# Performance work log

Hardware: AMD Instinct MI355X
Metric: run time of the kernel (lower is better)

The kernel has to match this reference:

```python
import jax, jax.numpy as jnp
import numpy as np

N_NODES = 50000
N_EDGES = 800000
D_IN = 1024
D_OUT = 256
LEAKY_SLOPE = 0.01  # F.leaky_relu default


def setup_inputs() -> dict:
    key = jax.random.key(0)
    k_x, k_w, k_b, k_src, k_dst, k_ew, k_norm = jax.random.split(key, 7)
    x = jax.random.normal(k_x, (N_NODES, D_IN), dtype=jnp.float32)
    # xavier_uniform-style scale for the weight
    limit = np.sqrt(6.0 / (D_IN + D_OUT)).astype(np.float32)
    weight = jax.random.uniform(k_w, (D_IN, D_OUT), dtype=jnp.float32, minval=-limit, maxval=limit)
    stdv = 1.0 / np.sqrt(D_OUT)
    bias = jax.random.uniform(k_b, (D_OUT,), dtype=jnp.float32, minval=-stdv, maxval=stdv)
    src = jax.random.randint(k_src, (N_EDGES,), 0, N_NODES, dtype=jnp.int64)
    dst = jax.random.randint(k_dst, (N_EDGES,), 0, N_NODES, dtype=jnp.int64)
    edge_index = jnp.stack([src, dst], axis=0)  # [2, E]
    edge_weight = jax.random.uniform(k_ew, (N_EDGES,), dtype=jnp.float32)
    norm = jax.random.uniform(k_norm, (N_NODES, 1), dtype=jnp.float32) + 0.5  # avoid div-by-~0
    return {"x": x, "weight": weight, "bias": bias, "edge_index": edge_index,
            "edge_weight": edge_weight, "norm": norm}


def reference(x, weight, bias, edge_index, edge_weight, norm):
    # support = input @ W            [N, D_OUT]
    support = x @ weight
    src = edge_index[0]
    dst = edge_index[1]
    # spmm(adj, support): out[i] = sum_{e: dst_e == i} w_e * support[src_e]
    msgs = support[src] * edge_weight[:, None]            # [E, D_OUT]
    out = jax.ops.segment_sum(msgs, dst, num_segments=x.shape[0])  # [N, D_OUT]
    out = out / norm + bias
    return jax.nn.leaky_relu(out, negative_slope=LEAKY_SLOPE)
```

## Files before the change

### kernel.cpp

```cpp
#include <hip/hip_runtime.h>
#include <hip/hip_bf16.h>

#define N_NODES 50000
#define N_EDGES 800000
#define D_IN    1024
#define D_OUT   256
#define CAP     64
#define LEAKY   0.01f

typedef __attribute__((ext_vector_type(8))) short bf16x8;
typedef __attribute__((ext_vector_type(4))) float f32x4;
typedef __attribute__((ext_vector_type(4))) int   i32x4;
typedef unsigned short u16;

__device__ __forceinline__ u16 f2bfu(float f) {
  uint32_t x = __float_as_uint(f);
  uint32_t r = (x + 0x7FFFu + ((x >> 16) & 1u)) >> 16;
  return (u16)r;
}
__device__ __forceinline__ float bfu2f(u16 u) {
  return __uint_as_float(((uint32_t)u) << 16);
}
__device__ __forceinline__ int swz(int b) { return b ^ (((b >> 7) & 7) << 4); }
__device__ __forceinline__ int paddr(int r, int c) {
  return swz(((r) >> 1) * 128 + ((r) & 1) * 64 + (c));
}

__device__ __forceinline__ void gll16(const void* g, void* l) {
  __builtin_amdgcn_global_load_lds(
      (const __attribute__((address_space(1))) uint32_t*)g,
      (__attribute__((address_space(3))) uint32_t*)l, 16, 0, 0);
}

__global__ __launch_bounds__(256) void wconv_kernel(const float* __restrict__ w,
                                                    char* __restrict__ img,
                                                    int* __restrict__ deg) {
  const int t = blockIdx.x * 256 + threadIdx.x;
  if (t < N_NODES) deg[t] = 0;
  const int t2 = t + 32768;
  if (t2 < N_NODES) deg[t2] = 0;

  const int n   = t & 255;
  const int kc  = (t >> 8) * 8;
  const int kt  = kc >> 5;
  const int kin = kc & 31;
  bf16x8 v;
#pragma unroll
  for (int i = 0; i < 8; ++i) v[i] = (short)f2bfu(w[(size_t)(kc + i) * D_OUT + n]);
  *(bf16x8*)(img + kt * 16384 + paddr(n, kin * 2)) = v;
}

#define BMg 256
#define GEMM_BLOCKS ((N_NODES + BMg - 1) / BMg)
#define BUILD_BLOCKS 60

__global__ __launch_bounds__(512) void gemm_build_kernel(
    const float* __restrict__ x, const char* __restrict__ img,
    u16* __restrict__ support,
    const int* __restrict__ ei, const float* __restrict__ ew,
    int* __restrict__ deg, int2* __restrict__ csr) {
  __shared__ u16 Wbuf[3][8192];
  __shared__ u16 Xbuf[3][8192];

  if (blockIdx.x < BUILD_BLOCKS) {
    const int t0 = blockIdx.x * 512 + threadIdx.x;
    for (int e = t0; e < N_EDGES; e += BUILD_BLOCKS * 512) {
      const int src = ei[e];
      const int dst = ei[N_EDGES + e];
      const float w = ew[e];
      const int slot = atomicAdd(&deg[dst], 1);
      if (slot < CAP) csr[dst * CAP + slot] = make_int2(src, __float_as_int(w));
    }
    return;
  }

  const int tid  = threadIdx.x;
  const int lane = tid & 63;
  const int wid  = tid >> 6;
  const int wn   = wid & 1;
  const int wm   = wid >> 1;
  const int l15  = lane & 15;
  const int l16  = lane >> 4;
  const int m0   = (blockIdx.x - BUILD_BLOCKS) * BMg;

  f32x4 acc[8][4];
#pragma unroll
  for (int i = 0; i < 8; ++i)
#pragma unroll
    for (int j = 0; j < 4; ++j) acc[i][j] = (f32x4)0.0f;

  const int xrow = tid >> 1;
  const int xkc  = (tid & 1) * 16;
  const int xrg  = min(m0 + xrow, N_NODES - 1);
  const float* xp = x + (size_t)xrg * D_IN + xkc;
  const int xw0 = paddr(xrow, xkc * 2);
  const int xw1 = paddr(xrow, xkc * 2 + 16);

  int a_off[8], b_off[4];
#pragma unroll
  for (int nf = 0; nf < 8; ++nf)
    a_off[nf] = paddr(wn * 128 + nf * 16 + l15, l16 * 16);
#pragma unroll
  for (int mf = 0; mf < 4; ++mf)
    b_off[mf] = paddr(wm * 64 + mf * 16 + l15, l16 * 16);

  f32x4 xr[2][4];

#define XLOAD(set, tile) do {                                              \
    const int kcl_ = min((tile), 31);                                      \
    const float* p_ = xp + kcl_ * 32;                                      \
    xr[set][0] = __builtin_nontemporal_load((const f32x4*)(p_));           \
    xr[set][1] = __builtin_nontemporal_load((const f32x4*)(p_ + 4));       \
    xr[set][2] = __builtin_nontemporal_load((const f32x4*)(p_ + 8));       \
    xr[set][3] = __builtin_nontemporal_load((const f32x4*)(p_ + 12));      \
  } while (0)

#define GLL(sl, tile) do {                                                 \
    const int kcl_ = min((tile), 31);                                      \
    gll16(img + kcl_ * 16384 + tid * 16, (char*)&Wbuf[sl][0] + tid * 16);  \
    gll16(img + kcl_ * 16384 + 8192 + tid * 16,                            \
          (char*)&Wbuf[sl][0] + 8192 + tid * 16);                          \
  } while (0)

#define XCVT(set, sl) do {                                                 \
    bf16x8 v0_, v1_;                                                       \
    v0_[0] = (short)f2bfu(xr[set][0][0]); v0_[1] = (short)f2bfu(xr[set][0][1]); \
    v0_[2] = (short)f2bfu(xr[set][0][2]); v0_[3] = (short)f2bfu(xr[set][0][3]); \
    v0_[4] = (short)f2bfu(xr[set][1][0]); v0_[5] = (short)f2bfu(xr[set][1][1]); \
    v0_[6] = (short)f2bfu(xr[set][1][2]); v0_[7] = (short)f2bfu(xr[set][1][3]); \
    v1_[0] = (short)f2bfu(xr[set][2][0]); v1_[1] = (short)f2bfu(xr[set][2][1]); \
    v1_[2] = (short)f2bfu(xr[set][2][2]); v1_[3] = (short)f2bfu(xr[set][2][3]); \
    v1_[4] = (short)f2bfu(xr[set][3][0]); v1_[5] = (short)f2bfu(xr[set][3][1]); \
    v1_[6] = (short)f2bfu(xr[set][3][2]); v1_[7] = (short)f2bfu(xr[set][3][3]); \
    *(bf16x8*)((char*)&Xbuf[sl][0] + xw0) = v0_;                           \
    *(bf16x8*)((char*)&Xbuf[sl][0] + xw1) = v1_;                           \
  } while (0)

#define MFMA_TILE(sl) do {                                                 \
    bf16x8 af_[8], bf_[4];                                                 \
    _Pragma("unroll")                                                      \
    for (int nf_ = 0; nf_ < 8; ++nf_)                                      \
      af_[nf_] = *(const bf16x8*)((const char*)&Wbuf[sl][0] + a_off[nf_]); \
    _Pragma("unroll")                                                      \
    for (int mf_ = 0; mf_ < 4; ++mf_)                                      \
      bf_[mf_] = *(const bf16x8*)((const char*)&Xbuf[sl][0] + b_off[mf_]); \
    _Pragma("unroll")                                                      \
    for (int nf_ = 0; nf_ < 8; ++nf_)                                      \
      _Pragma("unroll")                                                    \
      for (int mf_ = 0; mf_ < 4; ++mf_)                                    \
        acc[nf_][mf_] = __builtin_amdgcn_mfma_f32_16x16x32_bf16(           \
            af_[nf_], bf_[mf_], acc[nf_][mf_], 0, 0, 0);                   \
  } while (0)

#define SYNC() do {                                                        \
    asm volatile("s_waitcnt vmcnt(6)" ::: "memory");                       \
    __builtin_amdgcn_sched_barrier(0);                                     \
    asm volatile("s_waitcnt lgkmcnt(0)" ::: "memory");                     \
    __builtin_amdgcn_s_barrier();                                          \
  } while (0)

#define BODY(sA, sB, sC, eN, eC, kt) do {                                  \
    MFMA_TILE(sA);                                                         \
    XCVT(eC, sB);                                                          \
    XLOAD(eN, (kt) + 2);                                                   \
    GLL(sC, (kt) + 2);                                                     \
    SYNC();                                                                \
  } while (0)

  XLOAD(0, 0);
  GLL(0, 0);
  XLOAD(1, 1);
  GLL(1, 1);
  XCVT(0, 0);
  asm volatile("s_waitcnt vmcnt(6)" ::: "memory");
  __builtin_amdgcn_sched_barrier(0);
  asm volatile("s_waitcnt lgkmcnt(0)" ::: "memory");
  __builtin_amdgcn_s_barrier();

  for (int kt = 0; kt < 30; kt += 6) {
    BODY(0, 1, 2, 0, 1, kt);
    BODY(1, 2, 0, 1, 0, kt + 1);
    BODY(2, 0, 1, 0, 1, kt + 2);
    BODY(0, 1, 2, 1, 0, kt + 3);
    BODY(1, 2, 0, 0, 1, kt + 4);
    BODY(2, 0, 1, 1, 0, kt + 5);
  }
  BODY(0, 1, 2, 0, 1, 30);
  BODY(1, 2, 0, 1, 0, 31);

#undef XLOAD
#undef GLL
#undef XCVT
#undef MFMA_TILE
#undef SYNC
#undef BODY

#pragma unroll
  for (int mf = 0; mf < 4; ++mf) {
    const int m = m0 + wm * 64 + mf * 16 + l15;
    if (m < N_NODES) {
#pragma unroll
      for (int nf = 0; nf < 8; ++nf) {
        const int n = wn * 128 + nf * 16 + l16 * 4;
        ushort4 o;
        o.x = f2bfu(acc[nf][mf][0]);
        o.y = f2bfu(acc[nf][mf][1]);
        o.z = f2bfu(acc[nf][mf][2]);
        o.w = f2bfu(acc[nf][mf][3]);
        *(ushort4*)&support[(size_t)m * D_OUT + n] = o;
      }
    }
  }
}

__global__ __launch_bounds__(256) void agg_kernel(const u16* __restrict__ support,
                                                  const int* __restrict__ deg,
                                                  const int2* __restrict__ csr,
                                                  const float* __restrict__ norm,
                                                  const float* __restrict__ bias,
                                                  float* __restrict__ out) {
  const int lane = threadIdx.x & 63;
  const int wid  = threadIdx.x >> 6;
  const int node = blockIdx.x * 4 + wid;
  const int d    = min(deg[node], CAP);
  const int cb   = node * CAP;
  const int ch   = lane * 4;

  float a0 = 0.f, a1 = 0.f, a2 = 0.f, a3 = 0.f;
  int s = 0;

  for (; s + 16 <= d; s += 16) {
    i32x4 q[8];
#pragma unroll
    for (int i = 0; i < 8; ++i)
      q[i] = __builtin_nontemporal_load((const i32x4*)&csr[cb + s + 2 * i]);
    ushort4 v[16];
#pragma unroll
    for (int i = 0; i < 8; ++i) {
      v[2 * i]     = *(const ushort4*)&support[(size_t)q[i][0] * D_OUT + ch];
      v[2 * i + 1] = *(const ushort4*)&support[(size_t)q[i][2] * D_OUT + ch];
    }
#pragma unroll
    for (int i = 0; i < 8; ++i) {
      const float wa = __int_as_float(q[i][1]);
      const float wb = __int_as_float(q[i][3]);
      a0 = fmaf(wa, bfu2f(v[2 * i].x), a0);
      a1 = fmaf(wa, bfu2f(v[2 * i].y), a1);
      a2 = fmaf(wa, bfu2f(v[2 * i].z), a2);
      a3 = fmaf(wa, bfu2f(v[2 * i].w), a3);
      a0 = fmaf(wb, bfu2f(v[2 * i + 1].x), a0);
      a1 = fmaf(wb, bfu2f(v[2 * i + 1].y), a1);
      a2 = fmaf(wb, bfu2f(v[2 * i + 1].z), a2);
      a3 = fmaf(wb, bfu2f(v[2 * i + 1].w), a3);
    }
  }

  for (; s + 8 <= d; s += 8) {
    i32x4 q[4];
#pragma unroll
    for (int i = 0; i < 4; ++i)
      q[i] = __builtin_nontemporal_load((const i32x4*)&csr[cb + s + 2 * i]);
    ushort4 v[8];
#pragma unroll
    for (int i = 0; i < 4; ++i) {
      v[2 * i]     = *(const ushort4*)&support[(size_t)q[i][0] * D_OUT + ch];
      v[2 * i + 1] = *(const ushort4*)&support[(size_t)q[i][2] * D_OUT + ch];
    }
#pragma unroll
    for (int i = 0; i < 4; ++i) {
      const float wa = __int_as_float(q[i][1]);
      const float wb = __int_as_float(q[i][3]);
      a0 = fmaf(wa, bfu2f(v[2 * i].x), a0);
      a1 = fmaf(wa, bfu2f(v[2 * i].y), a1);
      a2 = fmaf(wa, bfu2f(v[2 * i].z), a2);
      a3 = fmaf(wa, bfu2f(v[2 * i].w), a3);
      a0 = fmaf(wb, bfu2f(v[2 * i + 1].x), a0);
      a1 = fmaf(wb, bfu2f(v[2 * i + 1].y), a1);
      a2 = fmaf(wb, bfu2f(v[2 * i + 1].z), a2);
      a3 = fmaf(wb, bfu2f(v[2 * i + 1].w), a3);
    }
  }

  for (; s < d; ++s) {
    const int2  e   = csr[cb + s];
    const float wgt = __int_as_float(e.y);
    const ushort4 v = *(const ushort4*)&support[(size_t)e.x * D_OUT + ch];
    a0 = fmaf(wgt, bfu2f(v.x), a0);
    a1 = fmaf(wgt, bfu2f(v.y), a1);
    a2 = fmaf(wgt, bfu2f(v.z), a2);
    a3 = fmaf(wgt, bfu2f(v.w), a3);
  }

  const float rn = 1.0f / norm[node];
  const float4 b = *(const float4*)&bias[ch];
  float o0 = fmaf(a0, rn, b.x);
  float o1 = fmaf(a1, rn, b.y);
  float o2 = fmaf(a2, rn, b.z);
  float o3 = fmaf(a3, rn, b.w);
  o0 = o0 > 0.f ? o0 : o0 * LEAKY;
  o1 = o1 > 0.f ? o1 : o1 * LEAKY;
  o2 = o2 > 0.f ? o2 : o2 * LEAKY;
  o3 = o3 > 0.f ? o3 : o3 * LEAKY;
  f32x4 ov;
  ov[0] = o0; ov[1] = o1; ov[2] = o2; ov[3] = o3;
  __builtin_nontemporal_store(ov, (f32x4*)&out[(size_t)node * D_OUT + ch]);
}

extern "C" void kernel_launch(void* const* d_in, const int* in_sizes, int n_in,
                              void* d_out, int out_size, void* d_ws, size_t ws_size,
                              hipStream_t stream) {
  const float* x    = (const float*)d_in[0];
  const float* w    = (const float*)d_in[1];
  const float* bias = (const float*)d_in[2];
  const int*   ei   = (const int*)d_in[3];
  const float* ew   = (const float*)d_in[4];
  const float* norm = (const float*)d_in[5];
  float* out = (float*)d_out;

  char* ws = (char*)d_ws;
  u16*   support = (u16*)  (ws);
  char*  img     =         (ws + 25600000);
  int2*  csr     = (int2*) (ws + 26124288);
  int*   deg     = (int*)  (ws + 51724288);

  wconv_kernel<<<128, 256, 0, stream>>>(w, img, deg);
  gemm_build_kernel<<<BUILD_BLOCKS + GEMM_BLOCKS, 512, 0, stream>>>(
      x, img, support, ei, ew, deg, csr);
  agg_kernel<<<N_NODES / 4, 256, 0, stream>>>(support, deg, csr, norm, bias, out);
}
```

Baseline: 187.2 us.

## Restructure GEMM pipeline to 64-wide K tiles with double buffering and ping-pong barriers

Doubles the K tile from 32 to 64 and changes the weight image and LDS layout to match. The triple-buffered pipeline becomes a double buffer, and each tile's MFMA work is split into four quarters, each wrapped in s_barrier, s_setprio(1) and a second barrier. X loads are interleaved between the quarters. The aim is fewer synchronization rounds per K and better overlap of global loads with MFMA issue, at the cost of more barriers per tile, full vmcnt(0) waits, and more LDS (128KB total).

Measured after the change: 275.0 us. +46.9%, slower.

```diff
diff --git a/kernel.cpp b/kernel.cpp
--- a/kernel.cpp
+++ b/kernel.cpp
@@ -22,9 +22,6 @@
   return __uint_as_float(((uint32_t)u) << 16);
 }
 __device__ __forceinline__ int swz(int b) { return b ^ (((b >> 7) & 7) << 4); }
-__device__ __forceinline__ int paddr(int r, int c) {
-  return swz(((r) >> 1) * 128 + ((r) & 1) * 64 + (c));
-}
 
 __device__ __forceinline__ void gll16(const void* g, void* l) {
   __builtin_amdgcn_global_load_lds(
@@ -35,19 +32,19 @@
 __global__ __launch_bounds__(256) void wconv_kernel(const float* __restrict__ w,
                                                     char* __restrict__ img,
                                                     int* __restrict__ deg) {
-  const int t = blockIdx.x * 256 + threadIdx.x;
+  const int t   = blockIdx.x * 256 + threadIdx.x;
   if (t < N_NODES) deg[t] = 0;
   const int t2 = t + 32768;
   if (t2 < N_NODES) deg[t2] = 0;
 
   const int n   = t & 255;
   const int kc  = (t >> 8) * 8;
-  const int kt  = kc >> 5;
-  const int kin = kc & 31;
+  const int kt  = kc >> 6;
+  const int kin = kc & 63;
   bf16x8 v;
 #pragma unroll
   for (int i = 0; i < 8; ++i) v[i] = (short)f2bfu(w[(size_t)(kc + i) * D_OUT + n]);
-  *(bf16x8*)(img + kt * 16384 + paddr(n, kin * 2)) = v;
+  *(bf16x8*)(img + kt * 32768 + swz(n * 128 + kin * 2)) = v;
 }
 
 #define BMg 256
@@ -59,8 +56,8 @@
     u16* __restrict__ support,
     const int* __restrict__ ei, const float* __restrict__ ew,
     int* __restrict__ deg, int2* __restrict__ csr) {
-  __shared__ u16 Wbuf[3][8192];
-  __shared__ u16 Xbuf[3][8192];
+  __shared__ u16 Wb[2][16384];
+  __shared__ u16 Xb[2][16384];
 
   if (blockIdx.x < BUILD_BLOCKS) {
     const int t0 = blockIdx.x * 512 + threadIdx.x;
@@ -89,111 +86,129 @@
 #pragma unroll
     for (int j = 0; j < 4; ++j) acc[i][j] = (f32x4)0.0f;
 
-  const int xrow = tid >> 1;
-  const int xkc  = (tid & 1) * 16;
-  const int xrg  = min(m0 + xrow, N_NODES - 1);
-  const float* xp = x + (size_t)xrg * D_IN + xkc;
-  const int xw0 = paddr(xrow, xkc * 2);
-  const int xw1 = paddr(xrow, xkc * 2 + 16);
-
-  int a_off[8], b_off[4];
-#pragma unroll
-  for (int nf = 0; nf < 8; ++nf)
-    a_off[nf] = paddr(wn * 128 + nf * 16 + l15, l16 * 16);
-#pragma unroll
-  for (int mf = 0; mf < 4; ++mf)
-    b_off[mf] = paddr(wm * 64 + mf * 16 + l15, l16 * 16);
-
-  f32x4 xr[2][4];
-
-#define XLOAD(set, tile) do {                                              \
-    const int kcl_ = min((tile), 31);                                      \
-    const float* p_ = xp + kcl_ * 32;                                      \
-    xr[set][0] = __builtin_nontemporal_load((const f32x4*)(p_));           \
-    xr[set][1] = __builtin_nontemporal_load((const f32x4*)(p_ + 4));       \
-    xr[set][2] = __builtin_nontemporal_load((const f32x4*)(p_ + 8));       \
-    xr[set][3] = __builtin_nontemporal_load((const f32x4*)(p_ + 12));      \
-  } while (0)
-
-#define GLL(sl, tile) do {                                                 \
-    const int kcl_ = min((tile), 31);                                      \
-    gll16(img + kcl_ * 16384 + tid * 16, (char*)&Wbuf[sl][0] + tid * 16);  \
-    gll16(img + kcl_ * 16384 + 8192 + tid * 16,                            \
-          (char*)&Wbuf[sl][0] + 8192 + tid * 16);                          \
-  } while (0)
-
-#define XCVT(set, sl) do {                                                 \
-    bf16x8 v0_, v1_;                                                       \
-    v0_[0] = (short)f2bfu(xr[set][0][0]); v0_[1] = (short)f2bfu(xr[set][0][1]); \
-    v0_[2] = (short)f2bfu(xr[set][0][2]); v0_[3] = (short)f2bfu(xr[set][0][3]); \
-    v0_[4] = (short)f2bfu(xr[set][1][0]); v0_[5] = (short)f2bfu(xr[set][1][1]); \
-    v0_[6] = (short)f2bfu(xr[set][1][2]); v0_[7] = (short)f2bfu(xr[set][1][3]); \
-    v1_[0] = (short)f2bfu(xr[set][2][0]); v1_[1] = (short)f2bfu(xr[set][2][1]); \
-    v1_[2] = (short)f2bfu(xr[set][2][2]); v1_[3] = (short)f2bfu(xr[set][2][3]); \
-    v1_[4] = (short)f2bfu(xr[set][3][0]); v1_[5] = (short)f2bfu(xr[set][3][1]); \
-    v1_[6] = (short)f2bfu(xr[set][3][2]); v1_[7] = (short)f2bfu(xr[set][3][3]); \
-    *(bf16x8*)((char*)&Xbuf[sl][0] + xw0) = v0_;                           \
-    *(bf16x8*)((char*)&Xbuf[sl][0] + xw1) = v1_;                           \
-  } while (0)
-
-#define MFMA_TILE(sl) do {                                                 \
-    bf16x8 af_[8], bf_[4];                                                 \
+  const int xrow  = tid >> 1;
+  const int xhalf = (tid & 1) * 32;
+  const int xrg   = min(m0 + xrow, N_NODES - 1);
+  const float* xp = x + (size_t)xrg * D_IN + xhalf;
+  int xw[4];
+#pragma unroll
+  for (int j = 0; j < 4; ++j) xw[j] = swz(xrow * 128 + (xhalf + j * 8) * 2);
+
+  int a_off[2][8], b_off[2][4];
+#pragma unroll
+  for (int ks = 0; ks < 2; ++ks) {
+#pragma unroll
+    for (int nf = 0; nf < 8; ++nf)
+      a_off[ks][nf] = swz((wn * 128 + nf * 16 + l15) * 128 + ks * 64 + l16 * 16);
+#pragma unroll
+    for (int mf = 0; mf < 4; ++mf)
+      b_off[ks][mf] = swz((wm * 64 + mf * 16 + l15) * 128 + ks * 64 + l16 * 16);
+  }
+
+  f32x4 xs[8];
+  bf16x8 af[8];
+
+#define XLD(i0, tt) do {                                                   \
+    const int kc_ = min((tt), 15);                                         \
+    xs[i0]     = __builtin_nontemporal_load((const f32x4*)(xp + kc_ * 64));      \
+    xs[i0 + 1] = __builtin_nontemporal_load((const f32x4*)(xp + kc_ * 64 + 4));  \
+    xs[i0 + 2] = __builtin_nontemporal_load((const f32x4*)(xp + kc_ * 64 + 8));  \
+    xs[i0 + 3] = __builtin_nontemporal_load((const f32x4*)(xp + kc_ * 64 + 12)); \
+  } while (0)
+#define XLD2(i0, tt, fo) do {                                              \
+    const int kc_ = min((tt), 15);                                         \
+    xs[i0]     = __builtin_nontemporal_load((const f32x4*)(xp + kc_ * 64 + (fo)));      \
+    xs[i0 + 1] = __builtin_nontemporal_load((const f32x4*)(xp + kc_ * 64 + (fo) + 4));  \
+    xs[i0 + 2] = __builtin_nontemporal_load((const f32x4*)(xp + kc_ * 64 + (fo) + 8));  \
+    xs[i0 + 3] = __builtin_nontemporal_load((const f32x4*)(xp + kc_ * 64 + (fo) + 12)); \
+  } while (0)
+
+#define XCW(sl) do {                                                       \
+    _Pragma("unroll")                                                      \
+    for (int j_ = 0; j_ < 4; ++j_) {                                       \
+      bf16x8 v_;                                                           \
+      v_[0] = (short)f2bfu(xs[2 * j_][0]); v_[1] = (short)f2bfu(xs[2 * j_][1]); \
+      v_[2] = (short)f2bfu(xs[2 * j_][2]); v_[3] = (short)f2bfu(xs[2 * j_][3]); \
+      v_[4] = (short)f2bfu(xs[2 * j_ + 1][0]); v_[5] = (short)f2bfu(xs[2 * j_ + 1][1]); \
+      v_[6] = (short)f2bfu(xs[2 * j_ + 1][2]); v_[7] = (short)f2bfu(xs[2 * j_ + 1][3]); \
+      *(bf16x8*)((char*)&Xb[sl][0] + xw[j_]) = v_;                         \
+    }                                                                      \
+  } while (0)
+
+#define GLLW(sl, tt) do {                                                  \
+    const int kc_ = min((tt), 15);                                         \
+    _Pragma("unroll")                                                      \
+    for (int r_ = 0; r_ < 4; ++r_)                                         \
+      gll16(img + kc_ * 32768 + r_ * 8192 + tid * 16,                      \
+            (char*)&Wb[sl][0] + r_ * 8192 + tid * 16);                     \
+  } while (0)
+
+#define LDA(sl, ks) do {                                                   \
     _Pragma("unroll")                                                      \
     for (int nf_ = 0; nf_ < 8; ++nf_)                                      \
-      af_[nf_] = *(const bf16x8*)((const char*)&Wbuf[sl][0] + a_off[nf_]); \
+      af[nf_] = *(const bf16x8*)((const char*)&Wb[sl][0] + a_off[ks][nf_]); \
+  } while (0)
+
+#define MMQ(sl, ks, mp) do {                                               \
+    bf16x8 bf0_ = *(const bf16x8*)((const char*)&Xb[sl][0] + b_off[ks][2 * (mp)]); \
+    bf16x8 bf1_ = *(const bf16x8*)((const char*)&Xb[sl][0] + b_off[ks][2 * (mp) + 1]); \
+    __builtin_amdgcn_s_barrier();                                          \
+    asm volatile("s_waitcnt lgkmcnt(0)" ::: "memory");                     \
+    __builtin_amdgcn_sched_barrier(0);                                     \
+    __builtin_amdgcn_s_setprio(1);                                         \
     _Pragma("unroll")                                                      \
-    for (int mf_ = 0; mf_ < 4; ++mf_)                                      \
-      bf_[mf_] = *(const bf16x8*)((const char*)&Xbuf[sl][0] + b_off[mf_]); \
-    _Pragma("unroll")                                                      \
-    for (int nf_ = 0; nf_ < 8; ++nf_)                                      \
-      _Pragma("unroll")                                                    \
-      for (int mf_ = 0; mf_ < 4; ++mf_)                                    \
-        acc[nf_][mf_] = __builtin_amdgcn_mfma_f32_16x16x32_bf16(           \
-            af_[nf_], bf_[mf_], acc[nf_][mf_], 0, 0, 0);                   \
-  } while (0)
-
-#define SYNC() do {                                                        \
-    asm volatile("s_waitcnt vmcnt(6)" ::: "memory");                       \
+    for (int nf_ = 0; nf_ < 8; ++nf_) {                                    \
+      acc[nf_][2 * (mp)]     = __builtin_amdgcn_mfma_f32_16x16x32_bf16(    \
+          af[nf_], bf0_, acc[nf_][2 * (mp)], 0, 0, 0);                     \
+      acc[nf_][2 * (mp) + 1] = __builtin_amdgcn_mfma_f32_16x16x32_bf16(    \
+          af[nf_], bf1_, acc[nf_][2 * (mp) + 1], 0, 0, 0);                 \
+    }                                                                      \
+    __builtin_amdgcn_s_setprio(0);                                         \
+    __builtin_amdgcn_s_barrier();                                          \
+  } while (0)
+
+#define ITER(cur, nxt, T) do {                                             \
+        \
+    asm volatile("s_waitcnt vmcnt(0)" ::: "memory");                       \
     __builtin_amdgcn_sched_barrier(0);                                     \
-    asm volatile("s_waitcnt lgkmcnt(0)" ::: "memory");                     \
-    __builtin_amdgcn_s_barrier();                                          \
-  } while (0)
-
-#define BODY(sA, sB, sC, eN, eC, kt) do {                                  \
-    MFMA_TILE(sA);                                                         \
-    XCVT(eC, sB);                                                          \
-    XLOAD(eN, (kt) + 2);                                                   \
-    GLL(sC, (kt) + 2);                                                     \
-    SYNC();                                                                \
-  } while (0)
-
-  XLOAD(0, 0);
-  GLL(0, 0);
-  XLOAD(1, 1);
-  GLL(1, 1);
-  XCVT(0, 0);
-  asm volatile("s_waitcnt vmcnt(6)" ::: "memory");
+    XCW(nxt);                                                              \
+    GLLW(nxt, (T) + 1);                                                    \
+    LDA(cur, 0);                                                           \
+    MMQ(cur, 0, 0);                                                        \
+                                 \
+    XLD2(0, (T) + 2, 0);                                                   \
+    MMQ(cur, 0, 1);                                                        \
+                                 \
+    XLD2(4, (T) + 2, 16);                                                  \
+    LDA(cur, 1);                                                           \
+    MMQ(cur, 1, 0);                                                        \
+                                                  \
+    MMQ(cur, 1, 1);                                                        \
+  } while (0)
+
+  XLD2(0, 0, 0);
+  XLD2(4, 0, 16);
+  asm volatile("s_waitcnt vmcnt(0)" ::: "memory");
   __builtin_amdgcn_sched_barrier(0);
+  XCW(0);
+  GLLW(0, 0);
+  XLD2(0, 1, 0);
+  XLD2(4, 1, 16);
   asm volatile("s_waitcnt lgkmcnt(0)" ::: "memory");
   __builtin_amdgcn_s_barrier();
 
-  for (int kt = 0; kt < 30; kt += 6) {
-    BODY(0, 1, 2, 0, 1, kt);
-    BODY(1, 2, 0, 1, 0, kt + 1);
-    BODY(2, 0, 1, 0, 1, kt + 2);
-    BODY(0, 1, 2, 1, 0, kt + 3);
-    BODY(1, 2, 0, 0, 1, kt + 4);
-    BODY(2, 0, 1, 1, 0, kt + 5);
-  }
-  BODY(0, 1, 2, 0, 1, 30);
-  BODY(1, 2, 0, 1, 0, 31);
-
-#undef XLOAD
-#undef GLL
-#undef XCVT
-#undef MFMA_TILE
-#undef SYNC
-#undef BODY
+  for (int T = 0; T < 16; T += 2) {
+    ITER(0, 1, T);
+    ITER(1, 0, T + 1);
+  }
+
+#undef XLD
+#undef XLD2
+#undef XCW
+#undef GLLW
+#undef LDA
+#undef MMQ
+#undef ITER
 
 #pragma unroll
   for (int mf = 0; mf < 4; ++mf) {
```
